# Optimization experiments

Measured on AMD Instinct MI355X. Metric: run time of the kernel, lower is better.

Reference implementation:

```python
import jax, jax.numpy as jnp
import numpy as np

B, L, D = 4, 4096, 1024
DS, EXP, DC = 16, 2, 4
DI = EXP * D
K_SYM = max(3, 2 * DC + 1)  # 9


def _linear(x, w, b):
    # torch nn.Linear: y = x @ W^T + b, W:[out,in]
    return jnp.einsum('blc,oc->blo', x, w) + b


def _dwconv(x, kernel, bias, pad_l, pad_r):
    # x:[B,L,C], kernel:[C,1,k] depthwise, torch 'same' padding (asymmetric for even k)
    y = jax.lax.conv_general_dilated(
        x.transpose(0, 2, 1), kernel, window_strides=(1,),
        padding=[(pad_l, pad_r)], dimension_numbers=('NCH', 'OIH', 'NCH'),
        feature_group_count=x.shape[-1])
    return y.transpose(0, 2, 1) + bias


def _rmsnorm(x, w, eps=1e-6):
    scale = jax.lax.rsqrt(jnp.mean(x * x, axis=-1, keepdims=True) + eps)
    return w * x * scale


def setup_inputs() -> dict:
    key = jax.random.key(0)
    ks = jax.random.split(key, 12)
    def n(k, shape, s=0.02):
        return jax.random.normal(k, shape, jnp.float32) * s
    return {
        'x': jax.random.normal(ks[0], (B, L, D), jnp.float32),
        'norm_w': jnp.ones((D,), jnp.float32),
        'in_w': n(ks[1], (2 * DI, D)), 'in_b': jnp.zeros((2 * DI,), jnp.float32),
        'dwa_k': n(ks[2], (DI, 1, DC)), 'dwa_b': jnp.zeros((DI,), jnp.float32),
        'A': n(ks[3], (DI, DS)), 'Bm': n(ks[4], (DS, DI)),
        'sym_k': n(ks[5], (DI, 1, K_SYM)), 'sym_b': jnp.zeros((DI,), jnp.float32),
        'pw_w': n(ks[6], (DI, DI)), 'pw_b': jnp.zeros((DI,), jnp.float32),
        'ha_w': n(ks[7], (DI // 2, DI)), 'ha_b': jnp.zeros((DI // 2,), jnp.float32),
        'hb_w': n(ks[8], (DI // 2, DI)), 'hb_b': jnp.zeros((DI // 2,), jnp.float32),
        'fuse_w': n(ks[9], (DI, DI)), 'fuse_b': jnp.zeros((DI,), jnp.float32),
        'out_w': n(ks[10], (D, DI)), 'out_b': jnp.zeros((D,), jnp.float32),
    }


def reference(x, norm_w, in_w, in_b, dwa_k, dwa_b, A, Bm, sym_k, sym_b,
              pw_w, pw_b, ha_w, ha_b, hb_w, hb_b, fuse_w, fuse_b, out_w, out_b):
    residual = x
    h = _rmsnorm(x, norm_w)
    h = _linear(h, in_w, in_b)                       # [B,L,2*DI]
    gate, val = h[..., :DI], h[..., DI:]
    gate = jax.nn.sigmoid(gate)
    # mamba-like branch: depthwise conv (k=4, torch 'same' -> pad (1,2)) + low-rank A@B
    a = _dwconv(val, dwa_k, dwa_b, 1, 2)             # [B,L,DI]
    a = jnp.einsum('bld,ds->bls', a, A)              # [B,L,DS]
    a = jnp.einsum('bls,sd->bld', a, Bm)             # [B,L,DI]
    # symmetric conv branch: depthwise conv (k=9, pad (4,4)) -> silu -> pointwise linear
    b = _dwconv(val, sym_k, sym_b, K_SYM // 2, K_SYM // 2)
    b = jax.nn.silu(b)
    b = _linear(b, pw_w, pw_b)
    a = _linear(a, ha_w, ha_b)                       # [B,L,DI/2]
    b = _linear(b, hb_w, hb_b)                       # [B,L,DI/2]
    y = jnp.concatenate([a, b], axis=-1)             # [B,L,DI]
    y = _linear(y, fuse_w, fuse_b)
    y = gate * y
    y = _linear(y, out_w, out_b)                     # [B,L,D]
    return residual + y
```

## Files before the change

### kernel.cpp

```cpp
#include <hip/hip_runtime.h>
#include <hip/hip_bf16.h>
#include <stdint.h>

typedef __bf16 bf16;
typedef __bf16 bf16x8 __attribute__((ext_vector_type(8)));
typedef __bf16 bf16x4 __attribute__((ext_vector_type(4)));
typedef float  f32x4  __attribute__((ext_vector_type(4)));

#define LDS_PTR(p) ((__attribute__((address_space(3))) uint32_t*)(p))
#define GLB_PTR(p) ((const __attribute__((address_space(1))) uint32_t*)(p))

static constexpr int BATCH = 4, SEQ = 4096, DMODEL = 1024;
static constexpr int DI = 2048;
static constexpr int MTOK = BATCH * SEQ;

enum { EPI_SPLIT = 0, EPI_PLAIN = 1, EPI_GATEADD = 2, EPI_RES = 3 };

template <int EPI, bool SPLITK = false>
__global__ __launch_bounds__(256) void gemm_bt(
    const bf16* __restrict__ Aact, const bf16* __restrict__ W,
    const float* __restrict__ bias,
    bf16* __restrict__ out0, bf16* __restrict__ out1,
    const bf16* __restrict__ gate,
    float* __restrict__ outf, const float* __restrict__ resid,
    int N, int K, int ldC, int col_off)
{
  __shared__ __align__(16) bf16 sA[128 * 64];
  __shared__ __align__(16) bf16 sB[128 * 64];
  const int tid  = threadIdx.x;
  int n0, m0, kbeg, kend;
  size_t out_off = 0;
  if (SPLITK) {
    n0 = 0; m0 = blockIdx.y * 128;
    const int kh = K / gridDim.x;
    kbeg = blockIdx.x * kh; kend = kbeg + kh;
    out_off = (size_t)blockIdx.x * ((size_t)MTOK * 128);
  } else {
    const int nT  = gridDim.x;
    const int lin = blockIdx.y * nT + blockIdx.x;
    const int grp = lin / (8 * nT);
    const int within = lin - grp * (8 * nT);
    n0 = (within >> 3) * 128;
    m0 = (grp * 8 + (within & 7)) * 128;
    kbeg = 0; kend = K;
  }
  const int lane = tid & 63;
  const int wv   = tid >> 6;
  const int wr   = wv >> 1, wc = wv & 1;
  const int l15  = lane & 15, quad = lane >> 4;

  f32x4 acc[4][4];
#pragma unroll
  for (int i = 0; i < 4; ++i)
#pragma unroll
    for (int j = 0; j < 4; ++j) acc[i][j] = (f32x4){0.f, 0.f, 0.f, 0.f};

  int rr[4], cb[4];
#pragma unroll
  for (int j = 0; j < 4; ++j) {
    const int s = tid + j * 256;
    rr[j] = s >> 3;
    cb[j] = ((s & 7) ^ (rr[j] & 7)) * 16;
  }

  const char* gA = (const char*)(Aact + (size_t)m0 * K);
  const char* gW = (const char*)(W + (size_t)n0 * K);

  for (int k0 = kbeg; k0 < kend; k0 += 64) {
    if (k0 != kbeg) __syncthreads();
#pragma unroll
    for (int j = 0; j < 4; ++j)
      __builtin_amdgcn_global_load_lds(GLB_PTR(gA + ((size_t)rr[j] * K + k0) * 2 + cb[j]),
                                       LDS_PTR(sA + (tid + j * 256) * 8), 16, 0, 0);
#pragma unroll
    for (int j = 0; j < 4; ++j)
      __builtin_amdgcn_global_load_lds(GLB_PTR(gW + ((size_t)rr[j] * K + k0) * 2 + cb[j]),
                                       LDS_PTR(sB + (tid + j * 256) * 8), 16, 0, 0);
    __syncthreads();

#pragma unroll
    for (int h = 0; h < 2; ++h) {
      bf16x8 av[4], bv[4];
#pragma unroll
      for (int t = 0; t < 4; ++t) {
        const int Ra = wr * 64 + t * 16 + l15;
        const int Rb = wc * 64 + t * 16 + l15;
        const int cc = h * 4 + quad;
        av[t] = *(const bf16x8*)(sA + (Ra * 8 + (cc ^ (Ra & 7))) * 8);
        bv[t] = *(const bf16x8*)(sB + (Rb * 8 + (cc ^ (Rb & 7))) * 8);
      }
#pragma unroll
      for (int i = 0; i < 4; ++i)
#pragma unroll
        for (int j = 0; j < 4; ++j)
          acc[i][j] = __builtin_amdgcn_mfma_f32_16x16x32_bf16(av[i], bv[j], acc[i][j], 0, 0, 0);
    }
  }

  bf16* o0 = out0 + out_off;
#pragma unroll
  for (int i = 0; i < 4; ++i) {
    const int mbase = m0 + wr * 64 + i * 16 + quad * 4;
#pragma unroll
    for (int j = 0; j < 4; ++j) {
      const int n = n0 + wc * 64 + j * 16 + l15;
      const float bj = bias ? bias[n] : 0.f;
#pragma unroll
      for (int r = 0; r < 4; ++r) {
        const int mm = mbase + r;
        float v = acc[i][j][r] + bj;
        if (EPI == EPI_SPLIT) {
          if (n < DI) o0[(size_t)mm * DI + n] = (bf16)(1.f / (1.f + __expf(-v)));
          else        out1[(size_t)mm * DI + (n - DI)] = (bf16)v;
        } else if (EPI == EPI_PLAIN) {
          o0[(size_t)mm * ldC + col_off + n] = (bf16)v;
        } else if (EPI == EPI_GATEADD) {
          const size_t idx = (size_t)mm * ldC + n;
          float zz = (float)o0[idx];
          float g  = (float)gate[(size_t)mm * DI + n];
          o0[idx] = (bf16)((v + zz) * g);
        } else {
          outf[(size_t)mm * ldC + n] = v + resid[(size_t)mm * ldC + n];
        }
      }
    }
  }
}

__global__ __launch_bounds__(256) void rmsnorm_kernel(
    const float* __restrict__ x, const float* __restrict__ w, bf16* __restrict__ out)
{
  const int row = blockIdx.x;
  const int tid = threadIdx.x;
  const float4 xv = ((const float4*)(x + (size_t)row * DMODEL))[tid];
  float s = xv.x * xv.x + xv.y * xv.y + xv.z * xv.z + xv.w * xv.w;
#pragma unroll
  for (int o = 32; o; o >>= 1) s += __shfl_xor(s, o);
  __shared__ float red[4];
  if ((tid & 63) == 0) red[tid >> 6] = s;
  __syncthreads();
  const float tot = red[0] + red[1] + red[2] + red[3];
  const float scale = rsqrtf(tot * (1.f / DMODEL) + 1e-6f);
  const float4 wv = ((const float4*)w)[tid];
  bf16x4 o4 = { (bf16)(xv.x * wv.x * scale), (bf16)(xv.y * wv.y * scale),
                (bf16)(xv.z * wv.z * scale), (bf16)(xv.w * wv.w * scale) };
  *(bf16x4*)(out + (size_t)row * DMODEL + tid * 4) = o4;
}

static constexpr int TL2 = 64;
__global__ __launch_bounds__(256) void conv_kernel(
    const bf16* __restrict__ val,
    const float* __restrict__ sym_k, const float* __restrict__ sym_b,
    bf16* __restrict__ bbuf)
{
  const int d  = (blockIdx.y * 256 + threadIdx.x) * 4;
  const int b  = blockIdx.z;
  const int l0 = blockIdx.x * TL2;
  float wk[9][4], bs[4];
#pragma unroll
  for (int j = 0; j < 4; ++j) {
    bs[j] = sym_b[d + j];
#pragma unroll
    for (int k = 0; k < 9; ++k) wk[k][j] = sym_k[(d + j) * 9 + k];
  }
  const bf16* base = val + (size_t)b * SEQ * DI + d;

  float win[9][4];
#pragma unroll
  for (int j = 0; j < 8; ++j) {
    const int xr = l0 + j - 4;
    if (xr >= 0 && xr < SEQ) {
      bf16x4 v = *(const bf16x4*)(base + (size_t)xr * DI);
#pragma unroll
      for (int c = 0; c < 4; ++c) win[j][c] = (float)v[c];
    } else {
#pragma unroll
      for (int c = 0; c < 4; ++c) win[j][c] = 0.f;
    }
  }
  for (int t = 0; t < TL2; ++t) {
    const int xf = l0 + t + 4;
    if (xf < SEQ) {
      bf16x4 v = *(const bf16x4*)(base + (size_t)xf * DI);
#pragma unroll
      for (int c = 0; c < 4; ++c) win[8][c] = (float)v[c];
    } else {
#pragma unroll
      for (int c = 0; c < 4; ++c) win[8][c] = 0.f;
    }
    float sb[4];
#pragma unroll
    for (int c = 0; c < 4; ++c) sb[c] = bs[c];
#pragma unroll
    for (int k = 0; k < 9; ++k)
#pragma unroll
      for (int c = 0; c < 4; ++c) sb[c] += win[k][c] * wk[k][c];
    bf16x4 o;
#pragma unroll
    for (int c = 0; c < 4; ++c) o[c] = (bf16)(sb[c] / (1.f + __expf(-sb[c])));
    *(bf16x4*)(bbuf + ((size_t)b * SEQ + l0 + t) * DI + d) = o;
#pragma unroll
    for (int k = 0; k < 8; ++k)
#pragma unroll
      for (int c = 0; c < 4; ++c) win[k][c] = win[k + 1][c];
  }
}

__global__ __launch_bounds__(256) void prep_cvt_kernel(
    const float* __restrict__ in_w, const float* __restrict__ hb_w,
    const float* __restrict__ out_w,
    bf16* __restrict__ in_wbf, bf16* __restrict__ hb_bf, bf16* __restrict__ out_bf)
{
  const int b = blockIdx.x;
  const float* src; bf16* dst; size_t i;
  if (b < 4096)      { src = in_w;  dst = in_wbf; i = (size_t)b * 256 + threadIdx.x; }
  else if (b < 6144) { src = hb_w;  dst = hb_bf;  i = (size_t)(b - 4096) * 256 + threadIdx.x; }
  else               { src = out_w; dst = out_bf; i = (size_t)(b - 6144) * 256 + threadIdx.x; }
  const float4 v = ((const float4*)src)[i];
  bf16x4 o4 = { (bf16)v.x, (bf16)v.y, (bf16)v.z, (bf16)v.w };
  *(bf16x4*)(dst + 4 * i) = o4;
}

__global__ __launch_bounds__(256) void transpose_kernel(
    const float* __restrict__ in, bf16* __restrict__ out)
{
  __shared__ float s[32][33];
  const int tid = threadIdx.x;
  const int r = tid >> 5, x = tid & 31;
  const int c0 = blockIdx.y * 32, d0 = blockIdx.x * 32;
#pragma unroll
  for (int rr = r; rr < 32; rr += 8)
    s[rr][x] = in[(size_t)(c0 + rr) * 2048 + d0 + x];
  __syncthreads();
#pragma unroll
  for (int rr = r; rr < 32; rr += 8)
    out[(size_t)(d0 + rr) * 2048 + c0 + x] = (bf16)s[x][rr];
}

__global__ __launch_bounds__(256) void prep_small_kernel(
    const float* __restrict__ Bm, const float* __restrict__ ha_w,
    const float* __restrict__ dwa_b, const float* __restrict__ dwa_k,
    const float* __restrict__ A,
    const float* __restrict__ hb_w, const float* __restrict__ pw_b,
    const float* __restrict__ hb_b, const float* __restrict__ fuse_w,
    float* __restrict__ T1, float* __restrict__ cvec, float* __restrict__ b_H,
    bf16* __restrict__ Wp, bf16* __restrict__ Fb)
{
  const int b = blockIdx.x, tid = threadIdx.x;
  __shared__ float red[4][16];
  if (b < 1024) {
    const int o = b;
    float acc[16];
#pragma unroll
    for (int s = 0; s < 16; ++s) acc[s] = 0.f;
    for (int d = tid; d < 2048; d += 256) {
      const float w = ha_w[(size_t)o * 2048 + d];
#pragma unroll
      for (int s = 0; s < 16; ++s) acc[s] += Bm[s * 2048 + d] * w;
    }
    const int lane = tid & 63, wv = tid >> 6;
#pragma unroll
    for (int s = 0; s < 16; ++s) {
      float v = acc[s];
#pragma unroll
      for (int off = 32; off; off >>= 1) v += __shfl_xor(v, off);
      if (lane == s) red[wv][s] = v;
    }
    __syncthreads();
    if (tid < 16)
      T1[tid * 1024 + o] = red[0][tid] + red[1][tid] + red[2][tid] + red[3][tid];
  } else if (b == 1024) {
    float acc[16];
#pragma unroll
    for (int s = 0; s < 16; ++s) acc[s] = 0.f;
    for (int d = tid; d < 2048; d += 256) {
      const float w = dwa_b[d];
#pragma unroll
      for (int s = 0; s < 16; ++s) acc[s] += w * A[d * 16 + s];
    }
    const int lane = tid & 63, wv = tid >> 6;
#pragma unroll
    for (int s = 0; s < 16; ++s) {
      float v = acc[s];
#pragma unroll
      for (int off = 32; off; off >>= 1) v += __shfl_xor(v, off);
      if (lane == s) red[wv][s] = v;
    }
    __syncthreads();
    if (tid < 16) cvec[tid] = red[0][tid] + red[1][tid] + red[2][tid] + red[3][tid];
  } else if (b < 1029) {
    const int o = (b - 1025) * 256 + tid;
    float acc = hb_b[o];
    const float* hr = hb_w + (size_t)o * 2048;
    for (int c = 0; c < 2048; c += 4) {
      float4 h = *(const float4*)(hr + c);
      float4 p = *(const float4*)(pw_b + c);
      acc += h.x * p.x + h.y * p.y + h.z * p.z + h.w * p.w;
    }
    b_H[o] = acc;
  } else if (b < 1037) {
    const int d = (b - 1029) * 256 + tid;
    float kk[4], av[16];
#pragma unroll
    for (int k = 0; k < 4; ++k) kk[k] = dwa_k[d * 4 + k];
#pragma unroll
    for (int s = 0; s < 16; ++s) av[s] = A[d * 16 + s];
#pragma unroll
    for (int k = 0; k < 4; ++k)
#pragma unroll
      for (int s = 0; s < 16; ++s)
        Wp[(size_t)(k * 16 + s) * 2048 + d] = (bf16)(kk[k] * av[s]);
    for (int n = 64; n < 128; ++n) Wp[(size_t)n * 2048 + d] = (bf16)0.f;
  } else {
    const int idx = (b - 1037) * 256 + tid;
    const int n = idx >> 8, o4 = idx & 255;
    float4 v = ((const float4*)(fuse_w + (size_t)n * 2048 + 1024))[o4];
    bf16x4 o = { (bf16)v.x, (bf16)v.y, (bf16)v.z, (bf16)v.w };
    *(bf16x4*)(Fb + (size_t)n * 1024 + o4 * 4) = o;
  }
}

__global__ __launch_bounds__(256) void prep_fuse_kernel(
    const float* __restrict__ T1, const float* __restrict__ fuse_w,
    const float* __restrict__ fuse_b, const float* __restrict__ ha_b,
    const float* __restrict__ b_H,
    float* __restrict__ T2t, float* __restrict__ bias_z)
{
  const int b = blockIdx.x, tid = threadIdx.x;
  if (b < 128) {
    const int n = b * 16 + (tid >> 4);
    const int s = tid & 15;
    const float* fr = fuse_w + (size_t)n * 2048;
    const float* tr = T1 + s * 1024;
    float acc = 0.f;
    for (int o = 0; o < 1024; o += 4) {
      float4 f = *(const float4*)(fr + o);
      float4 t = *(const float4*)(tr + o);
      acc += f.x * t.x + f.y * t.y + f.z * t.z + f.w * t.w;
    }
    T2t[n * 16 + s] = acc;
  } else {
    const int n = (b - 128) * 256 + tid;
    float acc = fuse_b[n];
    const float* fr = fuse_w + (size_t)n * 2048;
    for (int o = 0; o < 1024; o += 4) {
      float4 fa = *(const float4*)(fr + o);
      float4 fb = *(const float4*)(fr + 1024 + o);
      float4 ha = *(const float4*)(ha_b + o);
      float4 bh = *(const float4*)(b_H + o);
      acc += fa.x * ha.x + fa.y * ha.y + fa.z * ha.z + fa.w * ha.w;
      acc += fb.x * bh.x + fb.y * bh.y + fb.z * bh.z + fb.w * bh.w;
    }
    bias_z[n] = acc;
  }
}

__global__ __launch_bounds__(256) void za_kernel(
    const bf16* __restrict__ P0, const bf16* __restrict__ P1,
    const float* __restrict__ T2t,
    const float* __restrict__ cvec, const float* __restrict__ bias_z,
    bf16* __restrict__ z)
{
  __shared__ float s16t[32][16];
  const int tid = threadIdx.x;
  const int tok0 = blockIdx.x * 32;
  for (int p = tid; p < 512; p += 256) {
    const int t = p >> 4, s = p & 15;
    const int tok = tok0 + t;
    const int l = tok & (SEQ - 1), bb = tok >> 12;
    float acc = cvec[s];
#pragma unroll
    for (int k = 0; k < 4; ++k) {
      const int r = l - 1 + k;
      if ((unsigned)r < (unsigned)SEQ) {
        const size_t idx = ((size_t)bb * SEQ + r) * 128 + k * 16 + s;
        acc += (float)P0[idx] + (float)P1[idx];
      }
    }
    s16t[t][s] = acc;
  }
  const int c0 = tid * 8;
  float t2[8][16], bz[8];
#pragma unroll
  for (int j = 0; j < 8; ++j) {
    bz[j] = bias_z[c0 + j];
#pragma unroll
    for (int q = 0; q < 4; ++q) {
      float4 v = ((const float4*)(T2t + (size_t)(c0 + j) * 16))[q];
      t2[j][q * 4 + 0] = v.x; t2[j][q * 4 + 1] = v.y;
      t2[j][q * 4 + 2] = v.z; t2[j][q * 4 + 3] = v.w;
    }
  }
  __syncthreads();
  for (int t = 0; t < 32; ++t) {
    float sv[16];
#pragma unroll
    for (int s = 0; s < 16; ++s) sv[s] = s16t[t][s];
    bf16x8 o;
#pragma unroll
    for (int j = 0; j < 8; ++j) {
      float a = bz[j];
#pragma unroll
      for (int s = 0; s < 16; ++s) a += sv[s] * t2[j][s];
      o[j] = (bf16)a;
    }
    *(bf16x8*)(z + (size_t)(tok0 + t) * 2048 + c0) = o;
  }
}

extern "C" void kernel_launch(void* const* d_in, const int* in_sizes, int n_in,
                              void* d_out, int out_size, void* d_ws, size_t ws_size,
                              hipStream_t stream)
{
  const float* x      = (const float*)d_in[0];
  const float* norm_w = (const float*)d_in[1];
  const float* in_w   = (const float*)d_in[2];
  const float* in_b   = (const float*)d_in[3];
  const float* dwa_k  = (const float*)d_in[4];
  const float* dwa_b  = (const float*)d_in[5];
  const float* Amat   = (const float*)d_in[6];
  const float* Bm     = (const float*)d_in[7];
  const float* sym_k  = (const float*)d_in[8];
  const float* sym_b  = (const float*)d_in[9];
  const float* pw_w   = (const float*)d_in[10];
  const float* pw_b   = (const float*)d_in[11];
  const float* ha_w   = (const float*)d_in[12];
  const float* ha_b   = (const float*)d_in[13];
  const float* hb_w   = (const float*)d_in[14];
  const float* hb_b   = (const float*)d_in[15];
  const float* fuse_w = (const float*)d_in[16];
  const float* fuse_b = (const float*)d_in[17];
  const float* out_w  = (const float*)d_in[18];
  const float* out_b  = (const float*)d_in[19];
  float* out = (float*)d_out;

  char* ws = (char*)d_ws;
  const size_t MB = 1u << 20, KB = 1u << 10;
  bf16*  in_wbf  = (bf16*)(ws + 0);
  bf16*  hnorm   = (bf16*)(ws + 8 * MB);
  bf16*  bsilu   = (bf16*)(ws + 0);
  bf16*  valp    = (bf16*)(ws + 64 * MB);
  bf16*  zbuf    = (bf16*)(ws + 64 * MB);
  bf16*  gatep   = (bf16*)(ws + 128 * MB);
  bf16*  Pbuf    = (bf16*)(ws + 192 * MB);
  bf16*  pwT_bf  = (bf16*)(ws + 200 * MB);
  bf16*  WB_bf   = (bf16*)(ws + 200 * MB);
  bf16*  hb_bf   = (bf16*)(ws + 208 * MB);
  bf16*  Fb_bf   = (bf16*)(ws + 208 * MB);
  bf16*  Ht_bf   = (bf16*)(ws + 212 * MB);
  bf16*  out_bf  = (bf16*)(ws + 216 * MB);
  float* T1      = (float*)(ws + 220 * MB);
  float* cvec    = (float*)(ws + 220 * MB + 64 * KB);
  float* b_H     = (float*)(ws + 220 * MB + 68 * KB);
  float* bias_z  = (float*)(ws + 220 * MB + 72 * KB);
  bf16*  Wp      = (bf16*)(ws + 220 * MB + 80 * KB);
  float* T2t     = (float*)(ws + 220 * MB + 592 * KB);

  prep_cvt_kernel<<<8192, 256, 0, stream>>>(in_w, hb_w, out_w, in_wbf, hb_bf, out_bf);
  transpose_kernel<<<dim3(64, 64), 256, 0, stream>>>(pw_w, pwT_bf);
  gemm_bt<EPI_PLAIN><<<dim3(8, 16), 256, 0, stream>>>(
      pwT_bf, hb_bf, nullptr, Ht_bf, nullptr, nullptr, nullptr, nullptr, 1024, 2048, 1024, 0);
  prep_small_kernel<<<3085, 256, 0, stream>>>(
      Bm, ha_w, dwa_b, dwa_k, Amat, hb_w, pw_b, hb_b, fuse_w,
      T1, cvec, b_H, Wp, Fb_bf);
  gemm_bt<EPI_PLAIN><<<dim3(16, 16), 256, 0, stream>>>(
      Fb_bf, Ht_bf, nullptr, WB_bf, nullptr, nullptr, nullptr, nullptr, 2048, 1024, 2048, 0);
  prep_fuse_kernel<<<136, 256, 0, stream>>>(T1, fuse_w, fuse_b, ha_b, b_H, T2t, bias_z);

  rmsnorm_kernel<<<MTOK, 256, 0, stream>>>(x, norm_w, hnorm);
  gemm_bt<EPI_SPLIT><<<dim3(32, 128), 256, 0, stream>>>(
      hnorm, in_wbf, in_b, gatep, valp, nullptr, nullptr, nullptr, 4096, 1024, DI, 0);
  conv_kernel<<<dim3(SEQ / TL2, 2, BATCH), 256, 0, stream>>>(
      valp, sym_k, sym_b, bsilu);
  gemm_bt<EPI_PLAIN, true><<<dim3(2, 128), 256, 0, stream>>>(
      valp, Wp, nullptr, Pbuf, nullptr, nullptr, nullptr, nullptr, 128, 2048, 128, 0);
  za_kernel<<<MTOK / 32, 256, 0, stream>>>(
      Pbuf, Pbuf + (size_t)MTOK * 128, T2t, cvec, bias_z, zbuf);
  gemm_bt<EPI_GATEADD><<<dim3(16, 128), 256, 0, stream>>>(
      bsilu, WB_bf, nullptr, zbuf, nullptr, gatep, nullptr, nullptr, 2048, 2048, 2048, 0);
  gemm_bt<EPI_RES><<<dim3(8, 128), 256, 0, stream>>>(
      zbuf, out_bf, out_b, nullptr, nullptr, nullptr, out, x, 1024, 2048, 1024, 0);
}
```

Baseline: 906.7 us.

## Add 256x256-tile 8-wave GEMM with phased LDS pipelining for main GEMMs

Introduces a new gemm256 kernel that uses 256x256 output tiles, 512 threads, double-buffered LDS filled by direct global-to-LDS loads, and four compute phases per K-step that interleave staging of the next tile with MFMA work under setprio. It also remaps blocks into groups of eight M-tiles for L2 reuse. The three large token GEMMs (input projection, gated fuse, output projection) switch to it. The goal is more operand reuse per LDS load and better overlap of memory with MFMA, at the cost of higher register and LDS use and fewer, larger blocks.

```diff
diff --git a/kernel.cpp b/kernel.cpp
--- a/kernel.cpp
+++ b/kernel.cpp
@@ -125,6 +125,163 @@
       }
     }
   }
+}
+
+template <int N> __device__ __forceinline__ void vmwait() {
+  if constexpr (N == 0)      asm volatile("s_waitcnt vmcnt(0)" ::: "memory");
+  else if constexpr (N == 2) asm volatile("s_waitcnt vmcnt(2)" ::: "memory");
+  else if constexpr (N == 4) asm volatile("s_waitcnt vmcnt(4)" ::: "memory");
+}
+
+#define G256_STAGE(gmat, smat, dstoff, half, k0)                                  \
+  do {                                                                            \
+    const char* _g = (gmat) + ((size_t)((half) * 128 + r0) * K + (size_t)(k0)) * 2 + c0; \
+    const int _d = (dstoff) + (half) * 8192 + tid * 8;                            \
+    __builtin_amdgcn_global_load_lds(GLB_PTR(_g), LDS_PTR((smat) + _d), 16, 0, 0); \
+    __builtin_amdgcn_global_load_lds(GLB_PTR(_g + (size_t)128 * K),               \
+                                     LDS_PTR((smat) + _d + 4096), 16, 0, 0);      \
+  } while (0)
+
+#define G256_PHASE(QR, QC, STM, STH, VM)                                          \
+  do {                                                                            \
+    bf16x8 av[2][4], bv[2][2];                                                    \
+    _Pragma("unroll")                                                             \
+    for (int kk = 0; kk < 2; ++kk) {                                              \
+      const int cc = kk * 4 + quad;                                               \
+      _Pragma("unroll")                                                           \
+      for (int i = 0; i < 4; ++i) {                                               \
+        const int R = (QR) * 128 + wr * 64 + i * 16 + l15;                        \
+        av[kk][i] = *(const bf16x8*)(sA + cur + (R >> 7) * 8192 +                 \
+                                     ((R & 127) * 8 + (cc ^ (R & 7))) * 8);       \
+      }                                                                           \
+      _Pragma("unroll")                                                           \
+      for (int j = 0; j < 2; ++j) {                                               \
+        const int R = (QC) * 128 + wc * 32 + j * 16 + l15;                        \
+        bv[kk][j] = *(const bf16x8*)(sB + cur + (R >> 7) * 8192 +                 \
+                                     ((R & 127) * 8 + (cc ^ (R & 7))) * 8);       \
+      }                                                                           \
+    }                                                                             \
+    if ((STM) == 0)      G256_STAGE(gA, sA, nxt, (STH), knext);                   \
+    else if ((STM) == 1) G256_STAGE(gW, sB, nxt, (STH), knext);                   \
+    vmwait<VM>();                                                                 \
+    __builtin_amdgcn_s_barrier();                                                 \
+    asm volatile("s_waitcnt lgkmcnt(0)" ::: "memory");                            \
+    __builtin_amdgcn_sched_barrier(0);                                            \
+    __builtin_amdgcn_s_setprio(1);                                                \
+    _Pragma("unroll")                                                             \
+    for (int kk = 0; kk < 2; ++kk)                                                \
+      _Pragma("unroll")                                                           \
+      for (int i = 0; i < 4; ++i)                                                 \
+        _Pragma("unroll")                                                         \
+        for (int j = 0; j < 2; ++j)                                               \
+          acc[QR][QC][i][j] = __builtin_amdgcn_mfma_f32_16x16x32_bf16(            \
+              av[kk][i], bv[kk][j], acc[QR][QC][i][j], 0, 0, 0);                  \
+    __builtin_amdgcn_s_setprio(0);                                                \
+    __builtin_amdgcn_sched_barrier(0);                                            \
+    __builtin_amdgcn_s_barrier();                                                 \
+    __builtin_amdgcn_sched_barrier(0);                                            \
+  } while (0)
+
+template <int EPI>
+__global__ __launch_bounds__(512, 2) void gemm256(
+    const bf16* __restrict__ Aact, const bf16* __restrict__ W,
+    const float* __restrict__ bias,
+    bf16* __restrict__ out0, bf16* __restrict__ out1,
+    const bf16* __restrict__ gate,
+    float* __restrict__ outf, const float* __restrict__ resid,
+    int K, int ldC)
+{
+  __shared__ __align__(16) bf16 sA[2 * 16384];
+  __shared__ __align__(16) bf16 sB[2 * 16384];
+  const int tid = threadIdx.x;
+
+  const int nT  = gridDim.x;
+  const int lin = blockIdx.y * nT + blockIdx.x;
+  const int grp = lin / (8 * nT);
+  const int within = lin - grp * (8 * nT);
+  const int n0 = (within >> 3) * 256;
+  const int m0 = (grp * 8 + (within & 7)) * 256;
+
+  const int lane = tid & 63;
+  const int wv   = tid >> 6;
+  const int wr   = wv >> 2;
+  const int wc   = wv & 3;
+  const int l15  = lane & 15, quad = lane >> 4;
+
+  f32x4 acc[2][2][4][2];
+#pragma unroll
+  for (int a = 0; a < 2; ++a)
+#pragma unroll
+    for (int b = 0; b < 2; ++b)
+#pragma unroll
+      for (int i = 0; i < 4; ++i)
+#pragma unroll
+        for (int j = 0; j < 2; ++j) acc[a][b][i][j] = (f32x4){0.f, 0.f, 0.f, 0.f};
+
+  const int r0 = tid >> 3;
+  const int c0 = ((tid & 7) ^ (r0 & 7)) * 16;
+
+  const char* gA = (const char*)(Aact + (size_t)m0 * K);
+  const char* gW = (const char*)(W + (size_t)n0 * K);
+
+  const int NT = K >> 6;
+
+  G256_STAGE(gA, sA, 0, 0, 0);
+  G256_STAGE(gA, sA, 0, 1, 0);
+  G256_STAGE(gW, sB, 0, 0, 0);
+  G256_STAGE(gW, sB, 0, 1, 0);
+  asm volatile("s_waitcnt vmcnt(0)" ::: "memory");
+  __builtin_amdgcn_s_barrier();
+
+  int cur = 0;
+  for (int t = 0; t < NT - 1; ++t) {
+    const int knext = (t + 1) * 64;
+    const int nxt = cur ^ 16384;
+    G256_PHASE(0, 0, 0, 0, 4);
+    G256_PHASE(1, 0, 1, 0, 4);
+    G256_PHASE(0, 1, 0, 1, 4);
+    G256_PHASE(1, 1, 1, 1, 4);
+    cur = nxt;
+  }
+  {
+    const int knext = 0;
+    const int nxt = cur;
+    (void)knext; (void)nxt;
+    G256_PHASE(0, 0, 2, 0, 2);
+    G256_PHASE(1, 0, 2, 0, 0);
+    G256_PHASE(0, 1, 2, 0, -1);
+    G256_PHASE(1, 1, 2, 0, -1);
+  }
+
+#pragma unroll
+  for (int qr = 0; qr < 2; ++qr)
+#pragma unroll
+    for (int qc = 0; qc < 2; ++qc)
+#pragma unroll
+      for (int i = 0; i < 4; ++i) {
+        const int mbase = m0 + qr * 128 + wr * 64 + i * 16 + quad * 4;
+#pragma unroll
+        for (int j = 0; j < 2; ++j) {
+          const int n = n0 + qc * 128 + wc * 32 + j * 16 + l15;
+          const float bj = bias ? bias[n] : 0.f;
+#pragma unroll
+          for (int r = 0; r < 4; ++r) {
+            const int mm = mbase + r;
+            float v = acc[qr][qc][i][j][r] + bj;
+            if (EPI == EPI_SPLIT) {
+              if (n < DI) out0[(size_t)mm * DI + n] = (bf16)(1.f / (1.f + __expf(-v)));
+              else        out1[(size_t)mm * DI + (n - DI)] = (bf16)v;
+            } else if (EPI == EPI_GATEADD) {
+              const size_t idx = (size_t)mm * ldC + n;
+              float zz = (float)out0[idx];
+              float g  = (float)gate[(size_t)mm * DI + n];
+              out0[idx] = (bf16)((v + zz) * g);
+            } else {
+              outf[(size_t)mm * ldC + n] = v + resid[(size_t)mm * ldC + n];
+            }
+          }
+        }
+      }
 }
 
 __global__ __launch_bounds__(256) void rmsnorm_kernel(
@@ -468,16 +625,16 @@
   prep_fuse_kernel<<<136, 256, 0, stream>>>(T1, fuse_w, fuse_b, ha_b, b_H, T2t, bias_z);
 
   rmsnorm_kernel<<<MTOK, 256, 0, stream>>>(x, norm_w, hnorm);
-  gemm_bt<EPI_SPLIT><<<dim3(32, 128), 256, 0, stream>>>(
-      hnorm, in_wbf, in_b, gatep, valp, nullptr, nullptr, nullptr, 4096, 1024, DI, 0);
+  gemm256<EPI_SPLIT><<<dim3(16, 64), 512, 0, stream>>>(
+      hnorm, in_wbf, in_b, gatep, valp, nullptr, nullptr, nullptr, 1024, DI);
   conv_kernel<<<dim3(SEQ / TL2, 2, BATCH), 256, 0, stream>>>(
       valp, sym_k, sym_b, bsilu);
   gemm_bt<EPI_PLAIN, true><<<dim3(2, 128), 256, 0, stream>>>(
       valp, Wp, nullptr, Pbuf, nullptr, nullptr, nullptr, nullptr, 128, 2048, 128, 0);
   za_kernel<<<MTOK / 32, 256, 0, stream>>>(
       Pbuf, Pbuf + (size_t)MTOK * 128, T2t, cvec, bias_z, zbuf);
-  gemm_bt<EPI_GATEADD><<<dim3(16, 128), 256, 0, stream>>>(
-      bsilu, WB_bf, nullptr, zbuf, nullptr, gatep, nullptr, nullptr, 2048, 2048, 2048, 0);
-  gemm_bt<EPI_RES><<<dim3(8, 128), 256, 0, stream>>>(
-      zbuf, out_bf, out_b, nullptr, nullptr, nullptr, out, x, 1024, 2048, 1024, 0);
-}
+  gemm256<EPI_GATEADD><<<dim3(8, 64), 512, 0, stream>>>(
+      bsilu, WB_bf, nullptr, zbuf, nullptr, gatep, nullptr, nullptr, 2048, 2048);
+  gemm256<EPI_RES><<<dim3(4, 64), 512, 0, stream>>>(
+      zbuf, out_bf, out_b, nullptr, nullptr, nullptr, out, x, 2048, 1024);
+}
```

After: 1.021 ms. 1.13x slower.

## Split-K the weight-prep GEMM, parallelize bias_z reduction, halve conv tile length

Applied to the files above, without the earlier changes.

The small 1024x1024x2048 weight-composition GEMM previously ran on only 128 blocks. It now uses split-K over 256 blocks writing fp32 partials, and the partials are summed into bf16 inside an extended prep_small_kernel. The bias_z computation moves from one thread per output looping over 1024 elements to one block per output using a wave-shuffle reduction. The conv tile length is halved to launch more blocks. Together these raise parallelism in the low-occupancy setup kernels, at the cost of extra fp32 partial traffic and more launches of small blocks.

```diff
diff --git a/kernel.cpp b/kernel.cpp
--- a/kernel.cpp
+++ b/kernel.cpp
@@ -14,7 +14,7 @@
 static constexpr int DI = 2048;
 static constexpr int MTOK = BATCH * SEQ;
 
-enum { EPI_SPLIT = 0, EPI_PLAIN = 1, EPI_GATEADD = 2, EPI_RES = 3 };
+enum { EPI_SPLIT = 0, EPI_PLAIN = 1, EPI_GATEADD = 2, EPI_RES = 3, EPI_F32S = 4 };
 
 template <int EPI, bool SPLITK = false>
 __global__ __launch_bounds__(256) void gemm_bt(
@@ -31,10 +31,12 @@
   int n0, m0, kbeg, kend;
   size_t out_off = 0;
   if (SPLITK) {
-    n0 = 0; m0 = blockIdx.y * 128;
+    n0 = blockIdx.z * 128;
+    m0 = blockIdx.y * 128;
     const int kh = K / gridDim.x;
     kbeg = blockIdx.x * kh; kend = kbeg + kh;
-    out_off = (size_t)blockIdx.x * ((size_t)MTOK * 128);
+    out_off = (EPI == EPI_F32S) ? (size_t)blockIdx.x * (size_t)col_off
+                                : (size_t)blockIdx.x * ((size_t)MTOK * 128);
   } else {
     const int nT  = gridDim.x;
     const int lin = blockIdx.y * nT + blockIdx.x;
@@ -97,7 +99,8 @@
     }
   }
 
-  bf16* o0 = out0 + out_off;
+  bf16*  o0 = out0 + out_off;
+  float* of = outf ? outf + out_off : nullptr;
 #pragma unroll
   for (int i = 0; i < 4; ++i) {
     const int mbase = m0 + wr * 64 + i * 16 + quad * 4;
@@ -119,6 +122,8 @@
           float zz = (float)o0[idx];
           float g  = (float)gate[(size_t)mm * DI + n];
           o0[idx] = (bf16)((v + zz) * g);
+        } else if (EPI == EPI_F32S) {
+          of[(size_t)mm * ldC + n] = v;
         } else {
           outf[(size_t)mm * ldC + n] = v + resid[(size_t)mm * ldC + n];
         }
@@ -147,7 +152,7 @@
   *(bf16x4*)(out + (size_t)row * DMODEL + tid * 4) = o4;
 }
 
-static constexpr int TL2 = 64;
+static constexpr int TL2 = 32;
 __global__ __launch_bounds__(256) void conv_kernel(
     const bf16* __restrict__ val,
     const float* __restrict__ sym_k, const float* __restrict__ sym_b,
@@ -243,8 +248,9 @@
     const float* __restrict__ A,
     const float* __restrict__ hb_w, const float* __restrict__ pw_b,
     const float* __restrict__ hb_b, const float* __restrict__ fuse_w,
+    const float* __restrict__ Hp,
     float* __restrict__ T1, float* __restrict__ cvec, float* __restrict__ b_H,
-    bf16* __restrict__ Wp, bf16* __restrict__ Fb)
+    bf16* __restrict__ Wp, bf16* __restrict__ Fb, bf16* __restrict__ Ht)
 {
   const int b = blockIdx.x, tid = threadIdx.x;
   __shared__ float red[4][16];
@@ -311,12 +317,19 @@
       for (int s = 0; s < 16; ++s)
         Wp[(size_t)(k * 16 + s) * 2048 + d] = (bf16)(kk[k] * av[s]);
     for (int n = 64; n < 128; ++n) Wp[(size_t)n * 2048 + d] = (bf16)0.f;
-  } else {
+  } else if (b < 3085) {
     const int idx = (b - 1037) * 256 + tid;
     const int n = idx >> 8, o4 = idx & 255;
     float4 v = ((const float4*)(fuse_w + (size_t)n * 2048 + 1024))[o4];
     bf16x4 o = { (bf16)v.x, (bf16)v.y, (bf16)v.z, (bf16)v.w };
     *(bf16x4*)(Fb + (size_t)n * 1024 + o4 * 4) = o;
+  } else {
+    const size_t e4 = (size_t)(b - 3085) * 256 + tid;
+    float4 p0 = ((const float4*)Hp)[e4];
+    float4 p1 = ((const float4*)(Hp + 2048 * 1024))[e4];
+    bf16x4 o = { (bf16)(p0.x + p1.x), (bf16)(p0.y + p1.y),
+                 (bf16)(p0.z + p1.z), (bf16)(p0.w + p1.w) };
+    *(bf16x4*)(Ht + e4 * 4) = o;
   }
 }
 
@@ -340,18 +353,21 @@
     }
     T2t[n * 16 + s] = acc;
   } else {
-    const int n = (b - 128) * 256 + tid;
-    float acc = fuse_b[n];
+    const int n = b - 128;
     const float* fr = fuse_w + (size_t)n * 2048;
-    for (int o = 0; o < 1024; o += 4) {
-      float4 fa = *(const float4*)(fr + o);
-      float4 fb = *(const float4*)(fr + 1024 + o);
-      float4 ha = *(const float4*)(ha_b + o);
-      float4 bh = *(const float4*)(b_H + o);
-      acc += fa.x * ha.x + fa.y * ha.y + fa.z * ha.z + fa.w * ha.w;
-      acc += fb.x * bh.x + fb.y * bh.y + fb.z * bh.z + fb.w * bh.w;
-    }
-    bias_z[n] = acc;
+    const int o = tid * 4;
+    float4 fa = *(const float4*)(fr + o);
+    float4 fb = *(const float4*)(fr + 1024 + o);
+    float4 ha = *(const float4*)(ha_b + o);
+    float4 bh = *(const float4*)(b_H + o);
+    float acc = fa.x * ha.x + fa.y * ha.y + fa.z * ha.z + fa.w * ha.w
+              + fb.x * bh.x + fb.y * bh.y + fb.z * bh.z + fb.w * bh.w;
+#pragma unroll
+    for (int off = 32; off; off >>= 1) acc += __shfl_xor(acc, off);
+    __shared__ float r4[4];
+    if ((tid & 63) == 0) r4[tid >> 6] = acc;
+    __syncthreads();
+    if (tid == 0) bias_z[n] = fuse_b[n] + r4[0] + r4[1] + r4[2] + r4[3];
   }
 }
 
@@ -439,6 +455,7 @@
   bf16*  in_wbf  = (bf16*)(ws + 0);
   bf16*  hnorm   = (bf16*)(ws + 8 * MB);
   bf16*  bsilu   = (bf16*)(ws + 0);
+  float* Hpart   = (float*)(ws + 64 * MB);
   bf16*  valp    = (bf16*)(ws + 64 * MB);
   bf16*  zbuf    = (bf16*)(ws + 64 * MB);
   bf16*  gatep   = (bf16*)(ws + 128 * MB);
@@ -458,14 +475,15 @@
 
   prep_cvt_kernel<<<8192, 256, 0, stream>>>(in_w, hb_w, out_w, in_wbf, hb_bf, out_bf);
   transpose_kernel<<<dim3(64, 64), 256, 0, stream>>>(pw_w, pwT_bf);
-  gemm_bt<EPI_PLAIN><<<dim3(8, 16), 256, 0, stream>>>(
-      pwT_bf, hb_bf, nullptr, Ht_bf, nullptr, nullptr, nullptr, nullptr, 1024, 2048, 1024, 0);
-  prep_small_kernel<<<3085, 256, 0, stream>>>(
-      Bm, ha_w, dwa_b, dwa_k, Amat, hb_w, pw_b, hb_b, fuse_w,
-      T1, cvec, b_H, Wp, Fb_bf);
+  gemm_bt<EPI_F32S, true><<<dim3(2, 16, 8), 256, 0, stream>>>(
+      pwT_bf, hb_bf, nullptr, nullptr, nullptr, nullptr, Hpart, nullptr,
+      1024, 2048, 1024, 2048 * 1024);
+  prep_small_kernel<<<5133, 256, 0, stream>>>(
+      Bm, ha_w, dwa_b, dwa_k, Amat, hb_w, pw_b, hb_b, fuse_w, Hpart,
+      T1, cvec, b_H, Wp, Fb_bf, Ht_bf);
   gemm_bt<EPI_PLAIN><<<dim3(16, 16), 256, 0, stream>>>(
       Fb_bf, Ht_bf, nullptr, WB_bf, nullptr, nullptr, nullptr, nullptr, 2048, 1024, 2048, 0);
-  prep_fuse_kernel<<<136, 256, 0, stream>>>(T1, fuse_w, fuse_b, ha_b, b_H, T2t, bias_z);
+  prep_fuse_kernel<<<2176, 256, 0, stream>>>(T1, fuse_w, fuse_b, ha_b, b_H, T2t, bias_z);
 
   rmsnorm_kernel<<<MTOK, 256, 0, stream>>>(x, norm_w, hnorm);
   gemm_bt<EPI_SPLIT><<<dim3(32, 128), 256, 0, stream>>>(
```

Result: faster. 882.7 us (-2.6%).
